# Optimization experiments

Measured on AMD Instinct MI355X. Metric: run time of the kernel, lower is better.

The kernel has to match this reference:

```python
import jax, jax.numpy as jnp
import numpy as np

D = 512
H = 8
DV = D // H  # 64
NEG_INF = -1e30


def setup_inputs() -> dict:
    key = jax.random.key(0)
    ks = jax.random.split(key, 10)
    B, S = 4, 2048
    x = jax.random.normal(ks[0], (B, D, S), dtype=jnp.float32)
    mask = jnp.ones((B, S), dtype=jnp.float32)
    s = 1.0 / np.sqrt(D)
    sv = 1.0 / np.sqrt(D)
    # per-head Linear(d -> dv) weights stacked: [H, dv, d] (torch Linear layout W @ x)
    Wq = jax.random.uniform(ks[1], (H, DV, D), jnp.float32, -s, s)
    bq = jax.random.uniform(ks[2], (H, DV), jnp.float32, -s, s)
    Wk = jax.random.uniform(ks[3], (H, DV, D), jnp.float32, -s, s)
    bk = jax.random.uniform(ks[4], (H, DV), jnp.float32, -s, s)
    Wv = jax.random.uniform(ks[5], (H, DV, D), jnp.float32, -s, s)
    bv = jax.random.uniform(ks[6], (H, DV), jnp.float32, -s, s)
    W0 = jax.random.uniform(ks[7], (D, D), jnp.float32, -sv, sv)
    b0 = jax.random.uniform(ks[8], (D,), jnp.float32, -sv, sv)
    return {"x": x, "mask": mask, "Wq": Wq, "bq": bq, "Wk": Wk, "bk": bk,
            "Wv": Wv, "bv": bv, "W0": W0, "b0": b0}


def reference(x, mask, Wq, bq, Wk, bk, Wv, bv, W0, b0):
    # x: [B, d, S] -> xt: [B, S, d]
    xt = jnp.transpose(x, (0, 2, 1))
    # fused per-head projections: [B, H, S, dv]
    q = jnp.einsum('bsd,hed->bhse', xt, Wq) + bq[None, :, None, :]
    k = jnp.einsum('bsd,hed->bhse', xt, Wk) + bk[None, :, None, :]
    v = jnp.einsum('bsd,hed->bhse', xt, Wv) + bv[None, :, None, :]
    dv = q.shape[-1]
    scores = jnp.einsum('bhse,bhte->bhst', q, k) * (1.0 / np.sqrt(dv))
    # mask_logits (QANet style): keep where mask==1, else -1e30; mask over key dim
    h_mask = mask[:, None, None, :]  # [B,1,1,S]
    scores = scores * h_mask + (1.0 - h_mask) * NEG_INF
    p = jax.nn.softmax(scores, axis=-1)
    # zero out fully-masked query rows via v_mask on query dim
    p = p * mask[:, None, :, None]
    out = jnp.einsum('bhst,bhte->bhse', p, v)  # [B,H,S,dv]
    # concat heads along feature dim -> [B, S, d]
    B, _, S, _ = out.shape
    heads = jnp.transpose(out, (0, 2, 1, 3)).reshape(B, S, -1)
    y = heads @ W0.T + b0  # output projection
    return jnp.transpose(y, (0, 2, 1))  # [B, d, S]
```

## Files before the change

### kernel.cpp

```cpp
#include <hip/hip_runtime.h>

#define B_  4
#define D_  512
#define H_  8
#define DV_ 64
#define S_  2048
#define LDT 72

typedef __bf16 bf16;
typedef bf16  bf16x8 __attribute__((ext_vector_type(8)));
typedef bf16  bf16x4 __attribute__((ext_vector_type(4)));
typedef float f32x4  __attribute__((ext_vector_type(4)));

#define MFMA(a, b, c) __builtin_amdgcn_mfma_f32_16x16x32_bf16((a), (b), (c), 0, 0, 0)

__global__ __launch_bounds__(256) void transpose_x(const float* __restrict__ x,
                                                   bf16* __restrict__ xb) {
    __shared__ float tile[32][33];
    const int bidx = blockIdx.x;
    const int sblk = bidx % (S_ / 32);
    const int dblk = (bidx / (S_ / 32)) % (D_ / 32);
    const int b    = bidx / ((S_ / 32) * (D_ / 32));
    const int d0 = dblk * 32, s0 = sblk * 32;
    const int tx = threadIdx.x & 31;
    const int ty = threadIdx.x >> 5;
    const float* xp = x + (size_t)b * D_ * S_;
#pragma unroll
    for (int i = 0; i < 32; i += 8)
        tile[ty + i][tx] = xp[(size_t)(d0 + ty + i) * S_ + s0 + tx];
    __syncthreads();
    bf16* xbp = xb + ((size_t)b * S_ + s0) * D_ + d0;
#pragma unroll
    for (int i = 0; i < 32; i += 8)
        xbp[(size_t)(ty + i) * D_ + tx] = (bf16)tile[tx][ty + i];
}

__global__ __launch_bounds__(256) void gemm_qkv(
    const bf16* __restrict__ A,
    const float* __restrict__ Wq, const float* __restrict__ Wk, const float* __restrict__ Wv,
    const float* __restrict__ bq, const float* __restrict__ bk, const float* __restrict__ bv,
    bf16* __restrict__ Q, bf16* __restrict__ K, bf16* __restrict__ Vt) {
    __shared__ bf16 As[128][LDT];
    __shared__ bf16 Bs[64][LDT];

    const int tid  = threadIdx.x;
    const int w    = tid >> 6, lane = tid & 63;
    const int m16  = lane & 15, quad = lane >> 4;

    const int nblk = blockIdx.x % 24;
    const int mblk = blockIdx.x / 24;
    const int m0 = mblk * 128;
    const int n0 = nblk * 64;
    const int proj = n0 >> 9;
    const int nr   = n0 & 511;
    const float* W    = (proj == 0) ? Wq : (proj == 1) ? Wk : Wv;
    const float* bias = (proj == 0) ? bq : (proj == 1) ? bk : bv;

    f32x4 acc[2][4];
#pragma unroll
    for (int i = 0; i < 2; ++i)
#pragma unroll
        for (int j = 0; j < 4; ++j) acc[i][j] = (f32x4){0.f, 0.f, 0.f, 0.f};

    for (int k0 = 0; k0 < D_; k0 += 64) {
        __syncthreads();
        {
            const int col = (tid & 7) * 8;
            const int row = tid >> 3;
#pragma unroll
            for (int p = 0; p < 4; ++p) {
                const int r = row + p * 32;
                *(bf16x8*)&As[r][col] = *(const bf16x8*)&A[(size_t)(m0 + r) * D_ + k0 + col];
            }
        }
        {
            const int col = (tid & 15) * 4;
            const int row = tid >> 4;
#pragma unroll
            for (int p = 0; p < 4; ++p) {
                const int r = row + p * 16;
                const float4 v = *(const float4*)&W[(size_t)(nr + r) * D_ + k0 + col];
                bf16x4 hv = {(bf16)v.x, (bf16)v.y, (bf16)v.z, (bf16)v.w};
                *(bf16x4*)&Bs[r][col] = hv;
            }
        }
        __syncthreads();
#pragma unroll
        for (int kk = 0; kk < 2; ++kk) {
            const bf16x8 a0 = *(const bf16x8*)&As[w * 32 + m16][kk * 32 + quad * 8];
            const bf16x8 a1 = *(const bf16x8*)&As[w * 32 + 16 + m16][kk * 32 + quad * 8];
#pragma unroll
            for (int nt = 0; nt < 4; ++nt) {
                const bf16x8 bfr = *(const bf16x8*)&Bs[nt * 16 + m16][kk * 32 + quad * 8];
                acc[0][nt] = MFMA(a0, bfr, acc[0][nt]);
                acc[1][nt] = MFMA(a1, bfr, acc[1][nt]);
            }
        }
    }

#pragma unroll
    for (int mt = 0; mt < 2; ++mt)
#pragma unroll
        for (int nt = 0; nt < 4; ++nt) {
            const int n = nr + nt * 16 + m16;
            const int h = n >> 6, e = n & 63;
            const float bia = bias[n];
#pragma unroll
            for (int r = 0; r < 4; ++r) {
                const int M = m0 + w * 32 + mt * 16 + quad * 4 + r;
                const int b = M >> 11, s = M & 2047;
                const bf16 hv = (bf16)(acc[mt][nt][r] + bia);
                if (proj == 0)
                    Q[(((size_t)b * H_ + h) * S_ + s) * DV_ + e] = hv;
                else if (proj == 1)
                    K[(((size_t)b * H_ + h) * S_ + s) * DV_ + e] = hv;
                else
                    Vt[(((size_t)b * H_ + h) * DV_ + e) * S_ + s] = hv;
            }
        }
}

#define RS 36
__global__ __launch_bounds__(256, 2) void flash_attn(
    const bf16* __restrict__ Q, const bf16* __restrict__ K, const bf16* __restrict__ Vt,
    const float* __restrict__ mask, bf16* __restrict__ heads) {
    __shared__ union SMem {
        bf16 Ps[4][64][RS];
        struct { float O[64][65]; float L[64]; } red;
    } sm;

    const int bidx = blockIdx.x;
    const int qblk = bidx & 31;
    const int h    = (bidx >> 5) & 7;
    const int b    = bidx >> 8;
    const int q0   = qblk * 64;

    const int tid = threadIdx.x;
    const int w = tid >> 6, lane = tid & 63;
    const int m16 = lane & 15, quad = lane >> 4;

    const bf16* Qp = Q  + ((size_t)b * H_ + h) * S_ * DV_;
    const bf16* Kp = K  + ((size_t)b * H_ + h) * S_ * DV_;
    const bf16* Vp = Vt + ((size_t)b * H_ + h) * DV_ * S_;
    const float* mp = mask + (size_t)b * S_;

    bf16x8 qf[4][2];
#pragma unroll
    for (int mt = 0; mt < 4; ++mt)
#pragma unroll
        for (int kk = 0; kk < 2; ++kk) {
            bf16x8 v = *(const bf16x8*)&Qp[(size_t)(q0 + mt * 16 + m16) * DV_ +
                                           kk * 32 + quad * 8];
#pragma unroll
            for (int i = 0; i < 8; ++i) v[i] = (bf16)((float)v[i] * 0.125f);
            qf[mt][kk] = v;
        }

    bf16x8 ones;
#pragma unroll
    for (int i = 0; i < 8; ++i) ones[i] = (bf16)1.0f;

    f32x4 o[4][4];
    f32x4 lacc[4];
#pragma unroll
    for (int mt = 0; mt < 4; ++mt)
#pragma unroll
        for (int nt = 0; nt < 4; ++nt) o[mt][nt] = (f32x4){0.f, 0.f, 0.f, 0.f};
#pragma unroll
    for (int nt = 0; nt < 4; ++nt) lacc[nt] = (f32x4){0.f, 0.f, 0.f, 0.f};

    for (int t0 = 0; t0 < S_; t0 += 128) {
        const int tw = t0 + w * 32;

        bf16x8 kf[2][2];
#pragma unroll
        for (int nt = 0; nt < 2; ++nt)
#pragma unroll
            for (int kk = 0; kk < 2; ++kk)
                kf[nt][kk] = *(const bf16x8*)&Kp[(size_t)(tw + nt * 16 + m16) * DV_ +
                                                 kk * 32 + quad * 8];

        f32x4 sc[4][2];
#pragma unroll
        for (int mt = 0; mt < 4; ++mt)
#pragma unroll
            for (int nt = 0; nt < 2; ++nt) sc[mt][nt] = (f32x4){0.f, 0.f, 0.f, 0.f};
#pragma unroll
        for (int kk = 0; kk < 2; ++kk)
#pragma unroll
            for (int mt = 0; mt < 4; ++mt)
#pragma unroll
                for (int nt = 0; nt < 2; ++nt)
                    sc[mt][nt] = MFMA(qf[mt][kk], kf[nt][kk], sc[mt][nt]);

        const float mk0 = mp[tw + m16],      mk1 = mp[tw + 16 + m16];
        const float ng0 = (1.0f - mk0) * -1e30f, ng1 = (1.0f - mk1) * -1e30f;
#pragma unroll
        for (int mt = 0; mt < 4; ++mt)
#pragma unroll
            for (int r = 0; r < 4; ++r) {
                const int row = mt * 16 + quad * 4 + r;
                sm.Ps[w][row][m16]      = (bf16)__expf(sc[mt][0][r] * mk0 + ng0);
                sm.Ps[w][row][16 + m16] = (bf16)__expf(sc[mt][1][r] * mk1 + ng1);
            }

        bf16x8 pf[4];
#pragma unroll
        for (int nt = 0; nt < 4; ++nt)
            pf[nt] = *(const bf16x8*)&sm.Ps[w][nt * 16 + m16][quad * 8];
#pragma unroll
        for (int mt = 0; mt < 4; ++mt) {
            const bf16x8 vf = *(const bf16x8*)&Vp[(size_t)(mt * 16 + m16) * S_ +
                                                  tw + quad * 8];
#pragma unroll
            for (int nt = 0; nt < 4; ++nt) o[mt][nt] = MFMA(vf, pf[nt], o[mt][nt]);
        }
#pragma unroll
        for (int nt = 0; nt < 4; ++nt) lacc[nt] = MFMA(ones, pf[nt], lacc[nt]);
    }

    __syncthreads();
#pragma unroll
    for (int ww = 0; ww < 4; ++ww) {
        if (w == ww) {
#pragma unroll
            for (int mt = 0; mt < 4; ++mt)
#pragma unroll
                for (int nt = 0; nt < 4; ++nt)
#pragma unroll
                    for (int r = 0; r < 4; ++r) {
                        float* slot = &sm.red.O[mt * 16 + quad * 4 + r][nt * 16 + m16];
                        *slot = (ww == 0) ? o[mt][nt][r] : (*slot + o[mt][nt][r]);
                    }
            if (quad == 0)
#pragma unroll
                for (int nt = 0; nt < 4; ++nt) {
                    float* ls = &sm.red.L[nt * 16 + m16];
                    *ls = (ww == 0) ? lacc[nt][0] : (*ls + lacc[nt][0]);
                }
        }
        __syncthreads();
    }

    const int ql = tid >> 2, ec = (tid & 3) * 16;
    const float l  = sm.red.L[ql];
    const float qm = mp[q0 + ql];
    const float inv = qm / l;
    bf16x8 hv[2];
#pragma unroll
    for (int c = 0; c < 2; ++c)
#pragma unroll
        for (int i = 0; i < 8; ++i)
            hv[c][i] = (bf16)(sm.red.O[ec + c * 8 + i][ql] * inv);
    bf16* dst = &heads[((size_t)b * S_ + q0 + ql) * D_ + h * DV_ + ec];
    *(bf16x8*)(dst)     = hv[0];
    *(bf16x8*)(dst + 8) = hv[1];
}

__global__ __launch_bounds__(256) void gemm_out(
    const bf16* __restrict__ A, const float* __restrict__ W0,
    const float* __restrict__ b0, float* __restrict__ out) {
    __shared__ bf16 As[128][LDT];
    __shared__ bf16 Bs[64][LDT];

    const int tid = threadIdx.x;
    const int w = tid >> 6, lane = tid & 63;
    const int m16 = lane & 15, quad = lane >> 4;

    const int nblk = blockIdx.x % 8;
    const int mblk = blockIdx.x / 8;
    const int m0 = mblk * 128, n0 = nblk * 64;

    f32x4 acc[2][4];
#pragma unroll
    for (int i = 0; i < 2; ++i)
#pragma unroll
        for (int j = 0; j < 4; ++j) acc[i][j] = (f32x4){0.f, 0.f, 0.f, 0.f};

    for (int k0 = 0; k0 < D_; k0 += 64) {
        __syncthreads();
        {
            const int col = (tid & 7) * 8;
            const int row = tid >> 3;
#pragma unroll
            for (int p = 0; p < 4; ++p) {
                const int r = row + p * 32;
                *(bf16x8*)&As[r][col] = *(const bf16x8*)&A[(size_t)(m0 + r) * D_ + k0 + col];
            }
        }
        {
            const int col = (tid & 15) * 4;
            const int row = tid >> 4;
#pragma unroll
            for (int p = 0; p < 4; ++p) {
                const int r = row + p * 16;
                const float4 v = *(const float4*)&W0[(size_t)(n0 + r) * D_ + k0 + col];
                bf16x4 hv = {(bf16)v.x, (bf16)v.y, (bf16)v.z, (bf16)v.w};
                *(bf16x4*)&Bs[r][col] = hv;
            }
        }
        __syncthreads();
#pragma unroll
        for (int kk = 0; kk < 2; ++kk) {
            const bf16x8 a0 = *(const bf16x8*)&As[w * 32 + m16][kk * 32 + quad * 8];
            const bf16x8 a1 = *(const bf16x8*)&As[w * 32 + 16 + m16][kk * 32 + quad * 8];
#pragma unroll
            for (int nt = 0; nt < 4; ++nt) {
                const bf16x8 bfr = *(const bf16x8*)&Bs[nt * 16 + m16][kk * 32 + quad * 8];
                acc[0][nt] = MFMA(a0, bfr, acc[0][nt]);
                acc[1][nt] = MFMA(a1, bfr, acc[1][nt]);
            }
        }
    }

#pragma unroll
    for (int mt = 0; mt < 2; ++mt)
#pragma unroll
        for (int nt = 0; nt < 4; ++nt) {
            const int n  = n0 + nt * 16 + m16;
            const int Mb = m0 + w * 32 + mt * 16 + quad * 4;
            const int b  = Mb >> 11, s = Mb & 2047;
            const float bia = b0[n];
            float4 vv;
            vv.x = acc[mt][nt][0] + bia;
            vv.y = acc[mt][nt][1] + bia;
            vv.z = acc[mt][nt][2] + bia;
            vv.w = acc[mt][nt][3] + bia;
            *(float4*)&out[((size_t)b * D_ + n) * S_ + s] = vv;
        }
}

extern "C" void kernel_launch(void* const* d_in, const int* in_sizes, int n_in,
                              void* d_out, int out_size, void* d_ws, size_t ws_size,
                              hipStream_t stream) {
    const float* x    = (const float*)d_in[0];
    const float* mask = (const float*)d_in[1];
    const float* Wq   = (const float*)d_in[2];
    const float* bq   = (const float*)d_in[3];
    const float* Wk   = (const float*)d_in[4];
    const float* bk   = (const float*)d_in[5];
    const float* Wv   = (const float*)d_in[6];
    const float* bv   = (const float*)d_in[7];
    const float* W0   = (const float*)d_in[8];
    const float* b0   = (const float*)d_in[9];
    float* out = (float*)d_out;

    char* ws = (char*)d_ws;
    const size_t SEG = (size_t)B_ * S_ * D_ * sizeof(bf16);
    bf16* xb    = (bf16*)(ws);
    bf16* Qb    = (bf16*)(ws + SEG);
    bf16* Kb    = (bf16*)(ws + 2 * SEG);
    bf16* Vt    = (bf16*)(ws + 3 * SEG);
    bf16* heads = xb;

    transpose_x<<<dim3(B_ * (D_ / 32) * (S_ / 32)), dim3(256), 0, stream>>>(x, xb);
    gemm_qkv<<<dim3((B_ * S_ / 128) * (1536 / 64)), dim3(256), 0, stream>>>(
        xb, Wq, Wk, Wv, bq, bk, bv, Qb, Kb, Vt);
    flash_attn<<<dim3(B_ * H_ * (S_ / 64)), dim3(256), 0, stream>>>(Qb, Kb, Vt, mask, heads);
    gemm_out<<<dim3((B_ * S_ / 128) * (D_ / 64)), dim3(256), 0, stream>>>(heads, W0, b0, out);
}
```

Baseline: 208.5 us.

## Pre-convert weights to bf16, use 128x128 LDS-DMA GEMM tiles, prefetch K/V in attention

Merges the x transpose with a one-time fp32-to-bf16 conversion of all four weight matrices into a single prep kernel. Both GEMMs move to 128x128 block tiles with a 2x2 wave layout, loaded through global_load_lds DMA straight into an MFMA-fragment-ordered LDS layout. The flash attention loop register-prefetches the next K and V fragments to hide global load latency. V is now stored with vectorized bf16x4 writes. The changes add workspace use and register pressure, and the larger tiles mean fewer blocks per GEMM.

```diff
diff --git a/kernel.cpp b/kernel.cpp
--- a/kernel.cpp
+++ b/kernel.cpp
@@ -5,7 +5,6 @@
 #define H_  8
 #define DV_ 64
 #define S_  2048
-#define LDT 72
 
 typedef __bf16 bf16;
 typedef bf16  bf16x8 __attribute__((ext_vector_type(8)));
@@ -14,108 +13,125 @@
 
 #define MFMA(a, b, c) __builtin_amdgcn_mfma_f32_16x16x32_bf16((a), (b), (c), 0, 0, 0)
 
-__global__ __launch_bounds__(256) void transpose_x(const float* __restrict__ x,
-                                                   bf16* __restrict__ xb) {
-    __shared__ float tile[32][33];
-    const int bidx = blockIdx.x;
-    const int sblk = bidx % (S_ / 32);
-    const int dblk = (bidx / (S_ / 32)) % (D_ / 32);
-    const int b    = bidx / ((S_ / 32) * (D_ / 32));
-    const int d0 = dblk * 32, s0 = sblk * 32;
-    const int tx = threadIdx.x & 31;
-    const int ty = threadIdx.x >> 5;
-    const float* xp = x + (size_t)b * D_ * S_;
-#pragma unroll
-    for (int i = 0; i < 32; i += 8)
-        tile[ty + i][tx] = xp[(size_t)(d0 + ty + i) * S_ + s0 + tx];
-    __syncthreads();
-    bf16* xbp = xb + ((size_t)b * S_ + s0) * D_ + d0;
-#pragma unroll
-    for (int i = 0; i < 32; i += 8)
-        xbp[(size_t)(ty + i) * D_ + tx] = (bf16)tile[tx][ty + i];
+#define GLOAD_LDS(g, l)                                                     \
+    __builtin_amdgcn_global_load_lds(                                       \
+        (const __attribute__((address_space(1))) void*)(g),                 \
+        (__attribute__((address_space(3))) void*)(l), 16, 0, 0)
+
+__global__ __launch_bounds__(256) void prep(
+    const float* __restrict__ x, const float* __restrict__ Wq,
+    const float* __restrict__ Wk, const float* __restrict__ Wv,
+    const float* __restrict__ W0, bf16* __restrict__ xb, bf16* __restrict__ Wb) {
+    const int bid = blockIdx.x;
+    if (bid < 4096) {
+        __shared__ float tile[32][33];
+        const int sblk = bid % 64;
+        const int dblk = (bid / 64) % 16;
+        const int b    = bid / 1024;
+        const int d0 = dblk * 32, s0 = sblk * 32;
+        const int tx = threadIdx.x & 31;
+        const int ty = threadIdx.x >> 5;
+        const float* xp = x + (size_t)b * D_ * S_;
+#pragma unroll
+        for (int i = 0; i < 32; i += 8)
+            tile[ty + i][tx] = xp[(size_t)(d0 + ty + i) * S_ + s0 + tx];
+        __syncthreads();
+        bf16* xbp = xb + ((size_t)b * S_ + s0) * D_ + d0;
+#pragma unroll
+        for (int i = 0; i < 32; i += 8)
+            xbp[(size_t)(ty + i) * D_ + tx] = (bf16)tile[tx][ty + i];
+    } else {
+        const int f0 = ((bid - 4096) * 256 + threadIdx.x) * 16;
+        const int src = f0 >> 18;
+        const int off = f0 & 262143;
+        const float* W = (src == 0) ? Wq : (src == 1) ? Wk : (src == 2) ? Wv : W0;
+        float4 v0 = *(const float4*)&W[off];
+        float4 v1 = *(const float4*)&W[off + 4];
+        float4 v2 = *(const float4*)&W[off + 8];
+        float4 v3 = *(const float4*)&W[off + 12];
+        bf16x8 h0 = {(bf16)v0.x, (bf16)v0.y, (bf16)v0.z, (bf16)v0.w,
+                     (bf16)v1.x, (bf16)v1.y, (bf16)v1.z, (bf16)v1.w};
+        bf16x8 h1 = {(bf16)v2.x, (bf16)v2.y, (bf16)v2.z, (bf16)v2.w,
+                     (bf16)v3.x, (bf16)v3.y, (bf16)v3.z, (bf16)v3.w};
+        *(bf16x8*)&Wb[f0]     = h0;
+        *(bf16x8*)&Wb[f0 + 8] = h1;
+    }
 }
 
 __global__ __launch_bounds__(256) void gemm_qkv(
-    const bf16* __restrict__ A,
-    const float* __restrict__ Wq, const float* __restrict__ Wk, const float* __restrict__ Wv,
-    const float* __restrict__ bq, const float* __restrict__ bk, const float* __restrict__ bv,
+    const bf16* __restrict__ A, const bf16* __restrict__ Wb,
+    const float* __restrict__ bq, const float* __restrict__ bk,
+    const float* __restrict__ bv,
     bf16* __restrict__ Q, bf16* __restrict__ K, bf16* __restrict__ Vt) {
-    __shared__ bf16 As[128][LDT];
-    __shared__ bf16 Bs[64][LDT];
-
-    const int tid  = threadIdx.x;
-    const int w    = tid >> 6, lane = tid & 63;
-    const int m16  = lane & 15, quad = lane >> 4;
-
-    const int nblk = blockIdx.x % 24;
-    const int mblk = blockIdx.x / 24;
-    const int m0 = mblk * 128;
-    const int n0 = nblk * 64;
+    __shared__ bf16 Asl[8192];
+    __shared__ bf16 Bsl[8192];
+
+    const int tid = threadIdx.x;
+    const int w = tid >> 6, lane = tid & 63;
+    const int m16 = lane & 15, quad = lane >> 4;
+    const int wr = w & 1, wc = w >> 1;
+
+    const int nblk = blockIdx.x % 12;
+    const int mblk = blockIdx.x / 12;
+    const int m0 = mblk * 128, n0 = nblk * 128;
+
+    f32x4 acc[4][4];
+#pragma unroll
+    for (int i = 0; i < 4; ++i)
+#pragma unroll
+        for (int j = 0; j < 4; ++j) acc[i][j] = (f32x4){0.f, 0.f, 0.f, 0.f};
+
+    for (int k0 = 0; k0 < D_; k0 += 64) {
+        __syncthreads();
+#pragma unroll
+        for (int i = 0; i < 4; ++i) {
+            const int c  = w * 4 + i;
+            const int mt = c >> 1, kk = c & 1;
+            const int row = mt * 16 + m16;
+            const int col = k0 + kk * 32 + quad * 8;
+            GLOAD_LDS(&A[(size_t)(m0 + row) * D_ + col],  &Asl[(c * 64 + lane) * 8]);
+            GLOAD_LDS(&Wb[(size_t)(n0 + row) * D_ + col], &Bsl[(c * 64 + lane) * 8]);
+        }
+        __syncthreads();
+#pragma unroll
+        for (int kk = 0; kk < 2; ++kk) {
+            bf16x8 af[4], bfv[4];
+#pragma unroll
+            for (int t = 0; t < 4; ++t) {
+                af[t]  = *(const bf16x8*)&Asl[(((wr * 4 + t) * 2 + kk) * 64 + lane) * 8];
+                bfv[t] = *(const bf16x8*)&Bsl[(((wc * 4 + t) * 2 + kk) * 64 + lane) * 8];
+            }
+#pragma unroll
+            for (int mt = 0; mt < 4; ++mt)
+#pragma unroll
+                for (int nt = 0; nt < 4; ++nt)
+                    acc[mt][nt] = MFMA(af[mt], bfv[nt], acc[mt][nt]);
+        }
+    }
+
     const int proj = n0 >> 9;
-    const int nr   = n0 & 511;
-    const float* W    = (proj == 0) ? Wq : (proj == 1) ? Wk : Wv;
     const float* bias = (proj == 0) ? bq : (proj == 1) ? bk : bv;
-
-    f32x4 acc[2][4];
-#pragma unroll
-    for (int i = 0; i < 2; ++i)
-#pragma unroll
-        for (int j = 0; j < 4; ++j) acc[i][j] = (f32x4){0.f, 0.f, 0.f, 0.f};
-
-    for (int k0 = 0; k0 < D_; k0 += 64) {
-        __syncthreads();
-        {
-            const int col = (tid & 7) * 8;
-            const int row = tid >> 3;
-#pragma unroll
-            for (int p = 0; p < 4; ++p) {
-                const int r = row + p * 32;
-                *(bf16x8*)&As[r][col] = *(const bf16x8*)&A[(size_t)(m0 + r) * D_ + k0 + col];
-            }
-        }
-        {
-            const int col = (tid & 15) * 4;
-            const int row = tid >> 4;
-#pragma unroll
-            for (int p = 0; p < 4; ++p) {
-                const int r = row + p * 16;
-                const float4 v = *(const float4*)&W[(size_t)(nr + r) * D_ + k0 + col];
-                bf16x4 hv = {(bf16)v.x, (bf16)v.y, (bf16)v.z, (bf16)v.w};
-                *(bf16x4*)&Bs[r][col] = hv;
-            }
-        }
-        __syncthreads();
-#pragma unroll
-        for (int kk = 0; kk < 2; ++kk) {
-            const bf16x8 a0 = *(const bf16x8*)&As[w * 32 + m16][kk * 32 + quad * 8];
-            const bf16x8 a1 = *(const bf16x8*)&As[w * 32 + 16 + m16][kk * 32 + quad * 8];
-#pragma unroll
-            for (int nt = 0; nt < 4; ++nt) {
-                const bf16x8 bfr = *(const bf16x8*)&Bs[nt * 16 + m16][kk * 32 + quad * 8];
-                acc[0][nt] = MFMA(a0, bfr, acc[0][nt]);
-                acc[1][nt] = MFMA(a1, bfr, acc[1][nt]);
-            }
-        }
-    }
-
-#pragma unroll
-    for (int mt = 0; mt < 2; ++mt)
+#pragma unroll
+    for (int mt = 0; mt < 4; ++mt)
 #pragma unroll
         for (int nt = 0; nt < 4; ++nt) {
-            const int n = nr + nt * 16 + m16;
-            const int h = n >> 6, e = n & 63;
-            const float bia = bias[n];
-#pragma unroll
-            for (int r = 0; r < 4; ++r) {
-                const int M = m0 + w * 32 + mt * 16 + quad * 4 + r;
-                const int b = M >> 11, s = M & 2047;
-                const bf16 hv = (bf16)(acc[mt][nt][r] + bia);
-                if (proj == 0)
-                    Q[(((size_t)b * H_ + h) * S_ + s) * DV_ + e] = hv;
-                else if (proj == 1)
-                    K[(((size_t)b * H_ + h) * S_ + s) * DV_ + e] = hv;
-                else
-                    Vt[(((size_t)b * H_ + h) * DV_ + e) * S_ + s] = hv;
+            const int nlin = n0 + wc * 64 + nt * 16 + m16;
+            const int nr = nlin & 511;
+            const int h = nr >> 6, e = nr & 63;
+            const float bia = bias[nr];
+            const int srow = m0 + wr * 64 + mt * 16 + quad * 4;
+            const int b = srow >> 11, s = srow & 2047;
+            if (proj == 2) {
+                bf16x4 hv;
+#pragma unroll
+                for (int r = 0; r < 4; ++r) hv[r] = (bf16)(acc[mt][nt][r] + bia);
+                *(bf16x4*)&Vt[(((size_t)b * H_ + h) * DV_ + e) * S_ + s] = hv;
+            } else {
+                bf16* dst = (proj == 0) ? Q : K;
+#pragma unroll
+                for (int r = 0; r < 4; ++r)
+                    dst[(((size_t)b * H_ + h) * S_ + s + r) * DV_ + e] =
+                        (bf16)(acc[mt][nt][r] + bia);
             }
         }
 }
@@ -169,16 +185,37 @@
 #pragma unroll
     for (int nt = 0; nt < 4; ++nt) lacc[nt] = (f32x4){0.f, 0.f, 0.f, 0.f};
 
+    bf16x8 kfc[2][2], vfc[4];
+    {
+        const int tw = w * 32;
+#pragma unroll
+        for (int nt = 0; nt < 2; ++nt)
+#pragma unroll
+            for (int kk = 0; kk < 2; ++kk)
+                kfc[nt][kk] = *(const bf16x8*)&Kp[(size_t)(tw + nt * 16 + m16) * DV_ +
+                                                  kk * 32 + quad * 8];
+#pragma unroll
+        for (int mt = 0; mt < 4; ++mt)
+            vfc[mt] = *(const bf16x8*)&Vp[(size_t)(mt * 16 + m16) * S_ + tw + quad * 8];
+    }
+
     for (int t0 = 0; t0 < S_; t0 += 128) {
         const int tw = t0 + w * 32;
-
-        bf16x8 kf[2][2];
-#pragma unroll
-        for (int nt = 0; nt < 2; ++nt)
-#pragma unroll
-            for (int kk = 0; kk < 2; ++kk)
-                kf[nt][kk] = *(const bf16x8*)&Kp[(size_t)(tw + nt * 16 + m16) * DV_ +
-                                                 kk * 32 + quad * 8];
+        const bool more = (t0 + 128) < S_;
+
+        bf16x8 kfn[2][2], vfn[4];
+        if (more) {
+            const int twn = tw + 128;
+#pragma unroll
+            for (int nt = 0; nt < 2; ++nt)
+#pragma unroll
+                for (int kk = 0; kk < 2; ++kk)
+                    kfn[nt][kk] = *(const bf16x8*)&Kp[(size_t)(twn + nt * 16 + m16) * DV_ +
+                                                      kk * 32 + quad * 8];
+#pragma unroll
+            for (int mt = 0; mt < 4; ++mt)
+                vfn[mt] = *(const bf16x8*)&Vp[(size_t)(mt * 16 + m16) * S_ + twn + quad * 8];
+        }
 
         f32x4 sc[4][2];
 #pragma unroll
@@ -191,9 +228,9 @@
             for (int mt = 0; mt < 4; ++mt)
 #pragma unroll
                 for (int nt = 0; nt < 2; ++nt)
-                    sc[mt][nt] = MFMA(qf[mt][kk], kf[nt][kk], sc[mt][nt]);
-
-        const float mk0 = mp[tw + m16],      mk1 = mp[tw + 16 + m16];
+                    sc[mt][nt] = MFMA(qf[mt][kk], kfc[nt][kk], sc[mt][nt]);
+
+        const float mk0 = mp[tw + m16],          mk1 = mp[tw + 16 + m16];
         const float ng0 = (1.0f - mk0) * -1e30f, ng1 = (1.0f - mk1) * -1e30f;
 #pragma unroll
         for (int mt = 0; mt < 4; ++mt)
@@ -209,14 +246,20 @@
         for (int nt = 0; nt < 4; ++nt)
             pf[nt] = *(const bf16x8*)&sm.Ps[w][nt * 16 + m16][quad * 8];
 #pragma unroll
-        for (int mt = 0; mt < 4; ++mt) {
-            const bf16x8 vf = *(const bf16x8*)&Vp[(size_t)(mt * 16 + m16) * S_ +
-                                                  tw + quad * 8];
-#pragma unroll
-            for (int nt = 0; nt < 4; ++nt) o[mt][nt] = MFMA(vf, pf[nt], o[mt][nt]);
-        }
+        for (int mt = 0; mt < 4; ++mt)
+#pragma unroll
+            for (int nt = 0; nt < 4; ++nt) o[mt][nt] = MFMA(vfc[mt], pf[nt], o[mt][nt]);
 #pragma unroll
         for (int nt = 0; nt < 4; ++nt) lacc[nt] = MFMA(ones, pf[nt], lacc[nt]);
+
+        if (more) {
+#pragma unroll
+            for (int nt = 0; nt < 2; ++nt)
+#pragma unroll
+                for (int kk = 0; kk < 2; ++kk) kfc[nt][kk] = kfn[nt][kk];
+#pragma unroll
+            for (int mt = 0; mt < 4; ++mt) vfc[mt] = vfn[mt];
+        }
     }
 
     __syncthreads();
@@ -258,75 +301,68 @@
 }
 
 __global__ __launch_bounds__(256) void gemm_out(
-    const bf16* __restrict__ A, const float* __restrict__ W0,
-    const float* __restrict__ b0, float* __restrict__ out) {
-    __shared__ bf16 As[128][LDT];
-    __shared__ bf16 Bs[64][LDT];
+    const bf16* __restrict__ A, const bf16* __restrict__ Wb,
+    const float* __restrict__ b0, float* __restrict__ outp) {
+    __shared__ bf16 Asl[8192];
+    __shared__ bf16 Bsl[8192];
 
     const int tid = threadIdx.x;
     const int w = tid >> 6, lane = tid & 63;
     const int m16 = lane & 15, quad = lane >> 4;
-
-    const int nblk = blockIdx.x % 8;
-    const int mblk = blockIdx.x / 8;
-    const int m0 = mblk * 128, n0 = nblk * 64;
-
-    f32x4 acc[2][4];
-#pragma unroll
-    for (int i = 0; i < 2; ++i)
+    const int wr = w & 1, wc = w >> 1;
+
+    const int nblk = blockIdx.x & 3;
+    const int mblk = blockIdx.x >> 2;
+    const int m0 = mblk * 128, n0 = nblk * 128;
+
+    f32x4 acc[4][4];
+#pragma unroll
+    for (int i = 0; i < 4; ++i)
 #pragma unroll
         for (int j = 0; j < 4; ++j) acc[i][j] = (f32x4){0.f, 0.f, 0.f, 0.f};
 
     for (int k0 = 0; k0 < D_; k0 += 64) {
         __syncthreads();
-        {
-            const int col = (tid & 7) * 8;
-            const int row = tid >> 3;
-#pragma unroll
-            for (int p = 0; p < 4; ++p) {
-                const int r = row + p * 32;
-                *(bf16x8*)&As[r][col] = *(const bf16x8*)&A[(size_t)(m0 + r) * D_ + k0 + col];
+#pragma unroll
+        for (int i = 0; i < 4; ++i) {
+            const int c  = w * 4 + i;
+            const int mt = c >> 1, kk = c & 1;
+            const int row = mt * 16 + m16;
+            const int col = k0 + kk * 32 + quad * 8;
+            GLOAD_LDS(&A[(size_t)(m0 + row) * D_ + col], &Asl[(c * 64 + lane) * 8]);
+            GLOAD_LDS(&Wb[(size_t)(1536 + n0 + row) * D_ + col], &Bsl[(c * 64 + lane) * 8]);
+        }
+        __syncthreads();
+#pragma unroll
+        for (int kk = 0; kk < 2; ++kk) {
+            bf16x8 af[4], bfv[4];
+#pragma unroll
+            for (int t = 0; t < 4; ++t) {
+                af[t]  = *(const bf16x8*)&Asl[(((wr * 4 + t) * 2 + kk) * 64 + lane) * 8];
+                bfv[t] = *(const bf16x8*)&Bsl[(((wc * 4 + t) * 2 + kk) * 64 + lane) * 8];
             }
-        }
-        {
-            const int col = (tid & 15) * 4;
-            const int row = tid >> 4;
-#pragma unroll
-            for (int p = 0; p < 4; ++p) {
-                const int r = row + p * 16;
-                const float4 v = *(const float4*)&W0[(size_t)(n0 + r) * D_ + k0 + col];
-                bf16x4 hv = {(bf16)v.x, (bf16)v.y, (bf16)v.z, (bf16)v.w};
-                *(bf16x4*)&Bs[r][col] = hv;
-            }
-        }
-        __syncthreads();
-#pragma unroll
-        for (int kk = 0; kk < 2; ++kk) {
-            const bf16x8 a0 = *(const bf16x8*)&As[w * 32 + m16][kk * 32 + quad * 8];
-            const bf16x8 a1 = *(const bf16x8*)&As[w * 32 + 16 + m16][kk * 32 + quad * 8];
-#pragma unroll
-            for (int nt = 0; nt < 4; ++nt) {
-                const bf16x8 bfr = *(const bf16x8*)&Bs[nt * 16 + m16][kk * 32 + quad * 8];
-                acc[0][nt] = MFMA(a0, bfr, acc[0][nt]);
-                acc[1][nt] = MFMA(a1, bfr, acc[1][nt]);
-            }
-        }
-    }
-
-#pragma unroll
-    for (int mt = 0; mt < 2; ++mt)
+#pragma unroll
+            for (int mt = 0; mt < 4; ++mt)
+#pragma unroll
+                for (int nt = 0; nt < 4; ++nt)
+                    acc[mt][nt] = MFMA(af[mt], bfv[nt], acc[mt][nt]);
+        }
+    }
+
+#pragma unroll
+    for (int mt = 0; mt < 4; ++mt)
 #pragma unroll
         for (int nt = 0; nt < 4; ++nt) {
-            const int n  = n0 + nt * 16 + m16;
-            const int Mb = m0 + w * 32 + mt * 16 + quad * 4;
-            const int b  = Mb >> 11, s = Mb & 2047;
+            const int n = n0 + wc * 64 + nt * 16 + m16;
             const float bia = b0[n];
+            const int srow = m0 + wr * 64 + mt * 16 + quad * 4;
+            const int b = srow >> 11, s = srow & 2047;
             float4 vv;
             vv.x = acc[mt][nt][0] + bia;
             vv.y = acc[mt][nt][1] + bia;
             vv.z = acc[mt][nt][2] + bia;
             vv.w = acc[mt][nt][3] + bia;
-            *(float4*)&out[((size_t)b * D_ + n) * S_ + s] = vv;
+            *(float4*)&outp[((size_t)b * D_ + n) * S_ + s] = vv;
         }
 }
 
@@ -351,11 +387,11 @@
     bf16* Qb    = (bf16*)(ws + SEG);
     bf16* Kb    = (bf16*)(ws + 2 * SEG);
     bf16* Vt    = (bf16*)(ws + 3 * SEG);
+    bf16* Wb    = (bf16*)(ws + 4 * SEG);
     bf16* heads = xb;
 
-    transpose_x<<<dim3(B_ * (D_ / 32) * (S_ / 32)), dim3(256), 0, stream>>>(x, xb);
-    gemm_qkv<<<dim3((B_ * S_ / 128) * (1536 / 64)), dim3(256), 0, stream>>>(
-        xb, Wq, Wk, Wv, bq, bk, bv, Qb, Kb, Vt);
+    prep<<<dim3(4096 + 256), dim3(256), 0, stream>>>(x, Wq, Wk, Wv, W0, xb, Wb);
+    gemm_qkv<<<dim3(64 * 12), dim3(256), 0, stream>>>(xb, Wb, bq, bk, bv, Qb, Kb, Vt);
     flash_attn<<<dim3(B_ * H_ * (S_ / 64)), dim3(256), 0, stream>>>(Qb, Kb, Vt, mask, heads);
-    gemm_out<<<dim3((B_ * S_ / 128) * (D_ / 64)), dim3(256), 0, stream>>>(heads, W0, b0, out);
-}
+    gemm_out<<<dim3(64 * 4), dim3(256), 0, stream>>>(heads, Wb, b0, out);
+}
```

After: 216.1 us. +3.6%, slower.
